# Performance work log

Measured on AMD Instinct MI355X. Metric: run time of the kernel, lower is better.

Reference implementation:

```python
import jax, jax.numpy as jnp
import numpy as np

N_HEAD = 16

def setup_inputs() -> dict:
    key = jax.random.key(0)
    ks = jax.random.split(key, 9)
    B, T, C = 4, 2048, 1024
    s = 0.02
    return {
        "x": jax.random.normal(ks[0], (B, T, C), dtype=jnp.float32),
        "Wq": jax.random.normal(ks[1], (C, C), dtype=jnp.float32) * s,
        "bq": jnp.zeros((C,), dtype=jnp.float32),
        "Wk": jax.random.normal(ks[2], (C, C), dtype=jnp.float32) * s,
        "bk": jnp.zeros((C,), dtype=jnp.float32),
        "Wv": jax.random.normal(ks[3], (C, C), dtype=jnp.float32) * s,
        "bv": jnp.zeros((C,), dtype=jnp.float32),
        "Wo": jax.random.normal(ks[4], (C, C), dtype=jnp.float32) * s,
        "bo": jnp.zeros((C,), dtype=jnp.float32),
    }

def reference(x, Wq, bq, Wk, bk, Wv, bv, Wo, bo):
    B, T, C = x.shape
    H = N_HEAD
    d = C // H
    # QKV projections (Linear: y = x @ W + b), split heads -> [B, H, T, d]
    def proj(W, b):
        return (x @ W + b).reshape(B, T, H, d).transpose(0, 2, 1, 3)
    q = proj(Wq, bq)
    k = proj(Wk, bk)
    v = proj(Wv, bv)
    scale = jnp.float32(d) ** -0.5
    scores = jnp.einsum("bhtd,bhsd->bhts", q, k) * scale  # [B,H,T,T]
    attn = jax.nn.softmax(scores, axis=-1)
    out = jnp.einsum("bhts,bhsd->bhtd", attn, v)  # [B,H,T,d]
    out = out.transpose(0, 2, 1, 3).reshape(B, T, C)
    return out @ Wo + bo
```

## Files before the change

kernel.cpp:

```cpp
#include <hip/hip_runtime.h>
#include <hip/hip_bf16.h>

typedef unsigned short u16;
typedef unsigned int   u32;

typedef __bf16 bf16x8 __attribute__((ext_vector_type(8)));
typedef float  f32x4  __attribute__((ext_vector_type(4)));

#define MFMA16(A, B, C) __builtin_amdgcn_mfma_f32_16x16x32_bf16(A, B, C, 0, 0, 0)

static __device__ __forceinline__ u16 f2bf(float f) {
  union { float f; u32 u; } v; v.f = f;
  u32 r = v.u + 0x7fffu + ((v.u >> 16) & 1u);
  return (u16)(r >> 16);
}

static __device__ __forceinline__ float exp2a(float x) {
  float r; asm("v_exp_f32 %0, %1" : "=v"(r) : "v"(x)); return r;
}
static __device__ __forceinline__ float max3f(float a, float b, float c) {
  float r; asm("v_max3_f32 %0, %1, %2, %3" : "=v"(r) : "v"(a), "v"(b), "v"(c)); return r;
}
static __device__ __forceinline__ u32 cvtpk(float lo, float hi) {
  u32 r; asm("v_cvt_pk_bf16_f32 %0, %1, %2" : "=v"(r) : "v"(lo), "v"(hi)); return r;
}

static __device__ __forceinline__ void async16(const void* g, void* l) {
  __builtin_amdgcn_global_load_lds((const __attribute__((address_space(1))) void*)g,
                                   (__attribute__((address_space(3))) void*)l, 16, 0, 0);
}

static __device__ __forceinline__ int permrow(int r) {
  return (r & 3) | (((r >> 3) & 1) << 2);
}

__global__ __launch_bounds__(256) void prep_k(const float* __restrict__ x, u16* __restrict__ xb,
                                              const float* __restrict__ Wq, const float* __restrict__ Wk,
                                              const float* __restrict__ Wv, const float* __restrict__ Wo,
                                              u16* __restrict__ WT) {
  __shared__ float tile[32][33];
  const int bid = blockIdx.x;
  if (bid < 8192) {
    size_t i = ((size_t)bid * 256 + threadIdx.x) * 4;
    float4 v = *(const float4*)(x + i);
    u32 lo = (u32)f2bf(v.x) | ((u32)f2bf(v.y) << 16);
    u32 hi = (u32)f2bf(v.z) | ((u32)f2bf(v.w) << 16);
    *(uint2*)(xb + i) = make_uint2(lo, hi);
  } else {
    const int rem = bid - 8192;
    const int z = rem >> 10;
    const int rr = rem & 1023;
    const int n0 = (rr & 31) * 32;
    const int k0 = (rr >> 5) * 32;
    const float* W = (z == 0) ? Wq : (z == 1) ? Wk : (z == 2) ? Wv : Wo;
    u16* out = WT + (size_t)z * 1048576;
    const int tx = threadIdx.x & 31, ty = threadIdx.x >> 5;
#pragma unroll
    for (int i = 0; i < 4; i++)
      tile[ty + i * 8][tx] = W[(size_t)(k0 + ty + i * 8) * 1024 + n0 + tx];
    __syncthreads();
#pragma unroll
    for (int i = 0; i < 4; i++)
      out[(size_t)(n0 + ty + i * 8) * 1024 + k0 + tx] = f2bf(tile[tx][ty + i * 8]);
  }
}

#define G_STAGE(NXT)                                                          \
  {                                                                           \
    async16(pgA0, &As[(NXT) * 16384 + (0 * 512 + tid) * 8]);                  \
    async16(pgA1, &As[(NXT) * 16384 + (1 * 512 + tid) * 8]);                  \
    async16(pgA2, &As[(NXT) * 16384 + (2 * 512 + tid) * 8]);                  \
    async16(pgA3, &As[(NXT) * 16384 + (3 * 512 + tid) * 8]);                  \
    async16(pgB0, &Bs[(NXT) * 8192 + (0 * 512 + tid) * 8]);                   \
    async16(pgB1, &Bs[(NXT) * 8192 + (1 * 512 + tid) * 8]);                   \
    pgA0 += 64; pgA1 += 64; pgA2 += 64; pgA3 += 64; pgB0 += 64; pgB1 += 64;   \
  }

#define COMPUTE_T(CUR)                                                        \
  _Pragma("unroll")                                                           \
  for (int kk = 0; kk < 2; ++kk) {                                            \
    const u16* pAk = kk ? pA1 : pA0;                                          \
    const u16* pBk = kk ? pB1 : pB0;                                          \
    bf16x8 a0 = *(const bf16x8*)(pAk + (CUR) * 16384);                        \
    bf16x8 a1 = *(const bf16x8*)(pAk + (CUR) * 16384 + 1024);                 \
    bf16x8 a2 = *(const bf16x8*)(pAk + (CUR) * 16384 + 2048);                 \
    bf16x8 a3 = *(const bf16x8*)(pAk + (CUR) * 16384 + 3072);                 \
    bf16x8 b0 = *(const bf16x8*)(pBk + (CUR) * 8192);                         \
    bf16x8 b1 = *(const bf16x8*)(pBk + (CUR) * 8192 + 1024);                  \
    bf16x8 b2 = *(const bf16x8*)(pBk + (CUR) * 8192 + 2048);                  \
    bf16x8 b3 = *(const bf16x8*)(pBk + (CUR) * 8192 + 3072);                  \
    __builtin_amdgcn_s_setprio(1);                                            \
    acc[0][0] = MFMA16(a0, b0, acc[0][0]); acc[0][1] = MFMA16(a0, b1, acc[0][1]); \
    acc[0][2] = MFMA16(a0, b2, acc[0][2]); acc[0][3] = MFMA16(a0, b3, acc[0][3]); \
    acc[1][0] = MFMA16(a1, b0, acc[1][0]); acc[1][1] = MFMA16(a1, b1, acc[1][1]); \
    acc[1][2] = MFMA16(a1, b2, acc[1][2]); acc[1][3] = MFMA16(a1, b3, acc[1][3]); \
    acc[2][0] = MFMA16(a2, b0, acc[2][0]); acc[2][1] = MFMA16(a2, b1, acc[2][1]); \
    acc[2][2] = MFMA16(a2, b2, acc[2][2]); acc[2][3] = MFMA16(a2, b3, acc[2][3]); \
    acc[3][0] = MFMA16(a3, b0, acc[3][0]); acc[3][1] = MFMA16(a3, b1, acc[3][1]); \
    acc[3][2] = MFMA16(a3, b2, acc[3][2]); acc[3][3] = MFMA16(a3, b3, acc[3][3]); \
    __builtin_amdgcn_s_setprio(0);                                            \
  }

#define GITER(CUR, WN, STG, NXT)                                              \
  {                                                                           \
    asm volatile("s_waitcnt vmcnt(" #WN ")" ::: "memory");                    \
    __builtin_amdgcn_s_barrier();                                             \
    __builtin_amdgcn_sched_barrier(0);                                        \
    if (STG) G_STAGE(NXT)                                                     \
    COMPUTE_T(CUR)                                                            \
  }

template <int MODE>
__global__ __launch_bounds__(512, 2) void gemm256_k(const u16* __restrict__ A, const u16* __restrict__ WTall,
                                                    const float* __restrict__ b0, const float* __restrict__ b1,
                                                    const float* __restrict__ b2,
                                                    u16* __restrict__ outb, float* __restrict__ outf) {
  __shared__ u16 As[3 * 16384];
  __shared__ u16 Bs[3 * 8192];
  const int tid = threadIdx.x;
  const int lane = tid & 63;
  const int wid = tid >> 6;
  const int wm = wid >> 1, wn = wid & 1;
  const int g = lane >> 4, cc = lane & 15;

  const int bid = blockIdx.x;
  const int xcd = bid & 7;
  const int idx = bid >> 3;
  const int m0 = (xcd * 4 + (idx & 3)) * 256;
  const int nb = (idx >> 2) * 128;
  const u16* Bg = WTall + (size_t)(MODE == 0 ? 0 : 3145728) + (size_t)nb * 1024;

  const u16* pgA0; const u16* pgA1; const u16* pgA2; const u16* pgA3;
  const u16* pgB0; const u16* pgB1;
  {
    const int u0 = tid, u1 = 512 + tid, u2 = 1024 + tid, u3 = 1536 + tid;
    pgA0 = A + (size_t)(m0 + (u0 >> 3)) * 1024 + (((u0 & 7) ^ ((u0 >> 3) & 7)) << 3);
    pgA1 = A + (size_t)(m0 + (u1 >> 3)) * 1024 + (((u1 & 7) ^ ((u1 >> 3) & 7)) << 3);
    pgA2 = A + (size_t)(m0 + (u2 >> 3)) * 1024 + (((u2 & 7) ^ ((u2 >> 3) & 7)) << 3);
    pgA3 = A + (size_t)(m0 + (u3 >> 3)) * 1024 + (((u3 & 7) ^ ((u3 >> 3) & 7)) << 3);
    pgB0 = Bg + (size_t)(u0 >> 3) * 1024 + (((u0 & 7) ^ ((u0 >> 3) & 7)) << 3);
    pgB1 = Bg + (size_t)(u1 >> 3) * 1024 + (((u1 & 7) ^ ((u1 >> 3) & 7)) << 3);
  }

  const int s0 = g ^ (cc & 7);
  const u16* pA0 = As + (wm * 64 + cc) * 64 + (s0 << 3);
  const u16* pA1 = As + (wm * 64 + cc) * 64 + ((s0 ^ 4) << 3);
  const u16* pB0 = Bs + (wn * 64 + cc) * 64 + (s0 << 3);
  const u16* pB1 = Bs + (wn * 64 + cc) * 64 + ((s0 ^ 4) << 3);

  f32x4 acc[4][4] = {};

  G_STAGE(0)
  G_STAGE(1)

  for (int to = 0; to < 12; to += 3) {
    GITER(0, 6, 1, 2)
    GITER(1, 6, 1, 0)
    GITER(2, 6, 1, 1)
  }
  GITER(0, 6, 1, 2)
  GITER(1, 6, 1, 0)
  GITER(2, 6, 0, 0)
  GITER(0, 0, 0, 0)

  const int z = (MODE == 0) ? (nb >> 10) : 0;
  const float* bias = (MODE == 0) ? (z == 0 ? b0 : (z == 1 ? b1 : b2)) : b0;
  const float scl = (MODE == 0 && z == 0) ? 0.18033688011112042f : 1.0f;

#pragma unroll
  for (int mi = 0; mi < 4; mi++) {
#pragma unroll
    for (int ni = 0; ni < 4; ni++) {
      const int ng = nb + wn * 64 + ni * 16 + cc;
      const int n = (MODE == 0) ? (ng & 1023) : ng;
      const float bn = bias[n];
      const int mb = m0 + wm * 64 + mi * 16 + g * 4;
      if (MODE == 0) {
        u16* o = outb + (size_t)z * 8388608;
        if (z == 2) {
          u16 h[4];
#pragma unroll
          for (int r = 0; r < 4; r++) h[r] = f2bf(acc[mi][ni][r] + bn);
          const size_t ix = ((size_t)(((mb >> 11) * 16 + (n >> 6)) * 64 + (n & 63))) * 2048 + (mb & 2047);
          *(uint2*)&o[ix] = make_uint2((u32)h[0] | ((u32)h[1] << 16), (u32)h[2] | ((u32)h[3] << 16));
        } else {
#pragma unroll
          for (int r = 0; r < 4; r++) {
            const int m = mb + r;
            const float val = (acc[mi][ni][r] + bn) * scl;
            o[((size_t)((m >> 11) * 16 + (n >> 6)) * 2048 + (m & 2047)) * 64 + (n & 63)] = f2bf(val);
          }
        }
      } else {
#pragma unroll
        for (int r = 0; r < 4; r++)
          outf[(size_t)(mb + r) * 1024 + n] = acc[mi][ni][r] + bn;
      }
    }
  }
}

#define SMAX(S0, S1, M, O, PF)                                                \
  {                                                                           \
    float pm_ = max3f(max3f(S0[0], S0[1], S0[2]),                             \
                      max3f(S0[3], S1[0], S1[1]), fmaxf(S1[2], S1[3]));       \
    if (__builtin_expect(!__all(pm_ <= M + 8.0f), 0)) {                       \
      pm_ = fmaxf(pm_, __shfl_xor(pm_, 16));                                  \
      pm_ = fmaxf(pm_, __shfl_xor(pm_, 32));                                  \
      const float mn_ = fmaxf(M, pm_);                                        \
      const float al_ = exp2a(M - mn_);                                       \
      _Pragma("unroll")                                                       \
      for (int r_ = 0; r_ < 4; ++r_) {                                        \
        const float ar_ = __shfl(al_, g * 4 + r_);                            \
        _Pragma("unroll")                                                     \
        for (int t_ = 0; t_ < 5; ++t_) O[t_][r_] *= ar_;                      \
      }                                                                       \
      M = mn_;                                                                \
    }                                                                         \
    const float e0_ = exp2a(S0[0] - M), e1_ = exp2a(S0[1] - M);               \
    const float e2_ = exp2a(S0[2] - M), e3_ = exp2a(S0[3] - M);               \
    const float e4_ = exp2a(S1[0] - M), e5_ = exp2a(S1[1] - M);               \
    const float e6_ = exp2a(S1[2] - M), e7_ = exp2a(S1[3] - M);               \
    union { u32 u[4]; bf16x8 v; } pu_;                                        \
    pu_.u[0] = cvtpk(e0_, e1_); pu_.u[1] = cvtpk(e2_, e3_);                   \
    pu_.u[2] = cvtpk(e4_, e5_); pu_.u[3] = cvtpk(e6_, e7_);                   \
    PF = pu_.v;                                                               \
  }

#define COMPUTE(KB, VB)                                                       \
  _Pragma("unroll")                                                           \
  for (int sub = 0; sub < 2; ++sub) {                                         \
    const u16* pV_ = sub ? pV1 : pV0;                                         \
    bf16x8 k00 = *(const bf16x8*)(pK0 + (KB)*4096 + sub*2048);                \
    bf16x8 k01 = *(const bf16x8*)(pK1 + (KB)*4096 + sub*2048);                \
    bf16x8 k10 = *(const bf16x8*)(pK0 + (KB)*4096 + sub*2048 + 256);          \
    bf16x8 k11 = *(const bf16x8*)(pK1 + (KB)*4096 + sub*2048 + 256);          \
    __builtin_amdgcn_s_setprio(1);                                            \
    f32x4 sA0 = {}, sA1 = {}, sB0 = {}, sB1 = {};                             \
    sA0 = MFMA16(k00, qfA[0], sA0); sA0 = MFMA16(k01, qfA[1], sA0);           \
    sB0 = MFMA16(k00, qfB[0], sB0); sB0 = MFMA16(k01, qfB[1], sB0);           \
    sA1 = MFMA16(k10, qfA[0], sA1); sA1 = MFMA16(k11, qfA[1], sA1);           \
    sB1 = MFMA16(k10, qfB[0], sB1); sB1 = MFMA16(k11, qfB[1], sB1);           \
    __builtin_amdgcn_s_setprio(0);                                            \
    bf16x8 pfA, pfB;                                                          \
    SMAX(sA0, sA1, mA, oA, pfA);                                              \
    SMAX(sB0, sB1, mB, oB, pfB);                                              \
    __builtin_amdgcn_s_setprio(1);                                            \
    _Pragma("unroll")                                                         \
    for (int t = 0; t < 4; ++t) {                                             \
      bf16x8 vf = *(const bf16x8*)(pV_ + (VB)*4096 + t*1024);                 \
      oA[t] = MFMA16(pfA, vf, oA[t]);                                         \
      oB[t] = MFMA16(pfB, vf, oB[t]);                                         \
    }                                                                         \
    oA[4] = MFMA16(pfA, vone, oA[4]);                                         \
    oB[4] = MFMA16(pfB, vone, oB[4]);                                         \
    __builtin_amdgcn_s_setprio(0);                                            \
  }

#define ASTEP(KB, VB, IT, WN, SK, SV, KSB, VSB)                               \
  {                                                                           \
    asm volatile("s_waitcnt vmcnt(" #WN ")" ::: "memory");                    \
    __builtin_amdgcn_s_barrier();                                             \
    __builtin_amdgcn_sched_barrier(0);                                        \
    if (SV) {                                                                 \
      const size_t vo_ = (size_t)((IT) + 1) * 64;                             \
      async16(vS0 + vo_, &Vs[(VSB) * 4096 + tid * 8]);                        \
      async16(vS1 + vo_, &Vs[(VSB) * 4096 + tid * 8 + 2048]);                 \
    }                                                                         \
    if (SK) {                                                                 \
      const size_t ko_ = (size_t)((IT) + 2) * 4096;                           \
      async16(kS0 + ko_, &Ks[(KSB) * 4096 + tid * 8]);                        \
      async16(kS1 + ko_, &Ks[(KSB) * 4096 + tid * 8 + 2048]);                 \
    }                                                                         \
    COMPUTE(KB, VB)                                                           \
  }

__global__ __launch_bounds__(256, 4) void attn_k(const u16* __restrict__ Qg, const u16* __restrict__ Kg,
                                                 const u16* __restrict__ Vtg, u16* __restrict__ ctx) {
  __shared__ u16 Ks[3 * 4096];
  __shared__ u16 Vs[2 * 4096];
  const int tid = threadIdx.x;
  const int lane = tid & 63;
  const int wid = tid >> 6;
  const int g = lane >> 4, cc = lane & 15;
  const int a_ = cc >> 2, b_ = cc & 3;

  const int bid = blockIdx.x;
  const int xcd = bid & 7, tt = bid >> 3;
  const int bh = xcd * 8 + (tt >> 4);
  const int q0 = (tt & 15) * 128 + wid * 16;
  const size_t base = (size_t)bh * 131072;

  bf16x8 qfA[2], qfB[2];
#pragma unroll
  for (int c2 = 0; c2 < 2; c2++) {
    qfA[c2] = *(const bf16x8*)(Qg + base + (size_t)(q0 + cc) * 64 + c2 * 32 + g * 8);
    qfB[c2] = *(const bf16x8*)(Qg + base + (size_t)(q0 + 64 + cc) * 64 + c2 * 32 + g * 8);
  }

  bf16x8 vone;
#pragma unroll
  for (int j = 0; j < 8; j++) vone[j] = (__bf16)1.0f;

  float mA = -30000.0f, mB = -30000.0f;
  f32x4 oA[5] = {}, oB[5] = {};

  const int cK = b_ | ((a_ & 1) << 2);
  const int slK = g ^ cK;
  const u16* pK0 = &Ks[(8 * a_ + b_) * 64 + (slK << 3)];
  const u16* pK1 = &Ks[(8 * a_ + b_) * 64 + ((slK ^ 4) << 3)];
  const int cV = b_ | (((cc >> 3) & 1) << 2);
  const u16* pV0 = &Vs[cc * 64 + ((g ^ cV) << 3)];
  const u16* pV1 = &Vs[cc * 64 + (((4 + g) ^ cV) << 3)];

  const int r0 = tid >> 3, r1 = r0 + 32;
  const int slot = tid & 7;
  const int sp0 = slot ^ permrow(r0), sp1 = slot ^ permrow(r1);
  const u16* kS0 = Kg + base + (size_t)r0 * 64 + (sp0 << 3);
  const u16* kS1 = Kg + base + (size_t)r1 * 64 + (sp1 << 3);
  const u16* vS0 = Vtg + base + (size_t)r0 * 2048 + (sp0 << 3);
  const u16* vS1 = Vtg + base + (size_t)r1 * 2048 + (sp1 << 3);

  async16(kS0, &Ks[tid * 8]);
  async16(kS1, &Ks[tid * 8 + 2048]);
  async16(vS0, &Vs[tid * 8]);
  async16(vS1, &Vs[tid * 8 + 2048]);
  async16(kS0 + 4096, &Ks[4096 + tid * 8]);
  async16(kS1 + 4096, &Ks[4096 + tid * 8 + 2048]);
  async16(vS0 + 64, &Vs[4096 + tid * 8]);
  async16(vS1 + 64, &Vs[4096 + tid * 8 + 2048]);

  ASTEP(0, 0, 0, 4, 1, 0, 2, 0)
  for (int itb = 1; itb <= 19; itb += 6) {
    ASTEP(1, 1, itb + 0, 2, 1, 1, 0, 0)
    ASTEP(2, 0, itb + 1, 2, 1, 1, 1, 1)
    ASTEP(0, 1, itb + 2, 2, 1, 1, 2, 0)
    ASTEP(1, 0, itb + 3, 2, 1, 1, 0, 1)
    ASTEP(2, 1, itb + 4, 2, 1, 1, 1, 0)
    ASTEP(0, 0, itb + 5, 2, 1, 1, 2, 1)
  }
  ASTEP(1, 1, 25, 2, 1, 1, 0, 0)
  ASTEP(2, 0, 26, 2, 1, 1, 1, 1)
  ASTEP(0, 1, 27, 2, 1, 1, 2, 0)
  ASTEP(1, 0, 28, 2, 1, 1, 0, 1)
  ASTEP(2, 1, 29, 2, 1, 1, 1, 0)
  ASTEP(0, 0, 30, 2, 0, 1, 0, 1)
  ASTEP(1, 1, 31, 0, 0, 0, 0, 0)

  const int b = bh >> 4, h = bh & 15;
#pragma unroll
  for (int r = 0; r < 4; r++) {
    {
      const float inv = __builtin_amdgcn_rcpf(oA[4][r]);
      const int q = q0 + g * 4 + r;
#pragma unroll
      for (int t = 0; t < 4; t++)
        ctx[((size_t)((b * 2048 + q) * 16 + h)) * 64 + t * 16 + cc] = f2bf(oA[t][r] * inv);
    }
    {
      const float inv = __builtin_amdgcn_rcpf(oB[4][r]);
      const int q = q0 + 64 + g * 4 + r;
#pragma unroll
      for (int t = 0; t < 4; t++)
        ctx[((size_t)((b * 2048 + q) * 16 + h)) * 64 + t * 16 + cc] = f2bf(oB[t][r] * inv);
    }
  }
}

extern "C" void kernel_launch(void* const* d_in, const int* in_sizes, int n_in,
                              void* d_out, int out_size, void* d_ws, size_t ws_size,
                              hipStream_t stream) {
  const float* x  = (const float*)d_in[0];
  const float* Wq = (const float*)d_in[1];
  const float* bq = (const float*)d_in[2];
  const float* Wk = (const float*)d_in[3];
  const float* bk = (const float*)d_in[4];
  const float* Wv = (const float*)d_in[5];
  const float* bv = (const float*)d_in[6];
  const float* Wo = (const float*)d_in[7];
  const float* bo = (const float*)d_in[8];
  float* out = (float*)d_out;

  char* w = (char*)d_ws;
  u16* xb   = (u16*)(w);
  u16* WT   = (u16*)(w + (16u << 20));
  u16* QKV  = (u16*)(w + (24u << 20));
  u16* ctxb = (u16*)(w + (72u << 20));

  prep_k<<<dim3(12288), dim3(256), 0, stream>>>(x, xb, Wq, Wk, Wv, Wo, WT);
  gemm256_k<0><<<dim3(768), dim3(512), 0, stream>>>(xb, WT, bq, bk, bv, QKV, nullptr);
  attn_k<<<dim3(1024), dim3(256), 0, stream>>>(QKV, QKV + 8388608, QKV + 2 * 8388608, ctxb);
  gemm256_k<1><<<dim3(256), dim3(512), 0, stream>>>(ctxb, WT, bo, nullptr, nullptr, nullptr, out);
}
```

Baseline: 176.2 us.

## Software-pipeline QK^T of next sub-tile with softmax and PV of current

```diff
diff --git a/kernel.cpp b/kernel.cpp
--- a/kernel.cpp
+++ b/kernel.cpp
@@ -227,28 +227,32 @@
     PF = pu_.v;                                                               \
   }
 
-#define COMPUTE(KB, VB)                                                       \
-  _Pragma("unroll")                                                           \
-  for (int sub = 0; sub < 2; ++sub) {                                         \
-    const u16* pV_ = sub ? pV1 : pV0;                                         \
-    bf16x8 k00 = *(const bf16x8*)(pK0 + (KB)*4096 + sub*2048);                \
-    bf16x8 k01 = *(const bf16x8*)(pK1 + (KB)*4096 + sub*2048);                \
-    bf16x8 k10 = *(const bf16x8*)(pK0 + (KB)*4096 + sub*2048 + 256);          \
-    bf16x8 k11 = *(const bf16x8*)(pK1 + (KB)*4096 + sub*2048 + 256);          \
+#define QKSUB(KB, SOFF, A0, A1, B0, B1)                                       \
+  {                                                                           \
+    bf16x8 k00 = *(const bf16x8*)(pK0 + (KB) * 4096 + (SOFF));                \
+    bf16x8 k01 = *(const bf16x8*)(pK1 + (KB) * 4096 + (SOFF));                \
+    bf16x8 k10 = *(const bf16x8*)(pK0 + (KB) * 4096 + (SOFF) + 256);          \
+    bf16x8 k11 = *(const bf16x8*)(pK1 + (KB) * 4096 + (SOFF) + 256);          \
     __builtin_amdgcn_s_setprio(1);                                            \
-    f32x4 sA0 = {}, sA1 = {}, sB0 = {}, sB1 = {};                             \
-    sA0 = MFMA16(k00, qfA[0], sA0); sA0 = MFMA16(k01, qfA[1], sA0);           \
-    sB0 = MFMA16(k00, qfB[0], sB0); sB0 = MFMA16(k01, qfB[1], sB0);           \
-    sA1 = MFMA16(k10, qfA[0], sA1); sA1 = MFMA16(k11, qfA[1], sA1);           \
-    sB1 = MFMA16(k10, qfB[0], sB1); sB1 = MFMA16(k11, qfB[1], sB1);           \
+    A0 = (f32x4){0.f, 0.f, 0.f, 0.f}; A1 = (f32x4){0.f, 0.f, 0.f, 0.f};      \
+    B0 = (f32x4){0.f, 0.f, 0.f, 0.f}; B1 = (f32x4){0.f, 0.f, 0.f, 0.f};      \
+    A0 = MFMA16(k00, qfA[0], A0); A0 = MFMA16(k01, qfA[1], A0);               \
+    B0 = MFMA16(k00, qfB[0], B0); B0 = MFMA16(k01, qfB[1], B0);               \
+    A1 = MFMA16(k10, qfA[0], A1); A1 = MFMA16(k11, qfA[1], A1);               \
+    B1 = MFMA16(k10, qfB[0], B1); B1 = MFMA16(k11, qfB[1], B1);               \
     __builtin_amdgcn_s_setprio(0);                                            \
+  }
+
+#define SMPV(A0, A1, B0, B1, VB, SUB)                                         \
+  {                                                                           \
     bf16x8 pfA, pfB;                                                          \
-    SMAX(sA0, sA1, mA, oA, pfA);                                              \
-    SMAX(sB0, sB1, mB, oB, pfB);                                              \
+    SMAX(A0, A1, mA, oA, pfA);                                                \
+    SMAX(B0, B1, mB, oB, pfB);                                                \
+    const u16* pV_ = (SUB) ? pV1 : pV0;                                       \
     __builtin_amdgcn_s_setprio(1);                                            \
     _Pragma("unroll")                                                         \
     for (int t = 0; t < 4; ++t) {                                             \
-      bf16x8 vf = *(const bf16x8*)(pV_ + (VB)*4096 + t*1024);                 \
+      bf16x8 vf = *(const bf16x8*)(pV_ + (VB) * 4096 + t * 1024);             \
       oA[t] = MFMA16(pfA, vf, oA[t]);                                         \
       oB[t] = MFMA16(pfB, vf, oB[t]);                                         \
     }                                                                         \
@@ -257,9 +261,9 @@
     __builtin_amdgcn_s_setprio(0);                                            \
   }
 
-#define ASTEP(KB, VB, IT, WN, SK, SV, KSB, VSB)                               \
-  {                                                                           \
-    asm volatile("s_waitcnt vmcnt(" #WN ")" ::: "memory");                    \
+#define ASTEP3(KB, KBN, VB, IT, WT, WM, SK, SV, KSB, VSB, DOQK)               \
+  {                                                                           \
+    asm volatile("s_waitcnt vmcnt(" #WT ")" ::: "memory");                    \
     __builtin_amdgcn_s_barrier();                                             \
     __builtin_amdgcn_sched_barrier(0);                                        \
     if (SV) {                                                                 \
@@ -272,7 +276,13 @@
       async16(kS0 + ko_, &Ks[(KSB) * 4096 + tid * 8]);                        \
       async16(kS1 + ko_, &Ks[(KSB) * 4096 + tid * 8 + 2048]);                 \
     }                                                                         \
-    COMPUTE(KB, VB)                                                           \
+    QKSUB((KB), 2048, yA0, yA1, yB0, yB1)                                     \
+    SMPV(xA0, xA1, xB0, xB1, VB, 0)                                           \
+    asm volatile("s_waitcnt vmcnt(" #WM ")" ::: "memory");                    \
+    __builtin_amdgcn_s_barrier();                                             \
+    __builtin_amdgcn_sched_barrier(0);                                        \
+    if (DOQK) QKSUB((KBN), 0, xA0, xA1, xB0, xB1)                             \
+    SMPV(yA0, yA1, yB0, yB1, VB, 1)                                           \
   }
 
 __global__ __launch_bounds__(256, 4) void attn_k(const u16* __restrict__ Qg, const u16* __restrict__ Kg,
@@ -304,6 +314,7 @@
 
   float mA = -30000.0f, mB = -30000.0f;
   f32x4 oA[5] = {}, oB[5] = {};
+  f32x4 xA0, xA1, xB0, xB1, yA0, yA1, yB0, yB1;
 
   const int cK = b_ | ((a_ & 1) << 2);
   const int slK = g ^ cK;
@@ -330,22 +341,27 @@
   async16(vS0 + 64, &Vs[4096 + tid * 8]);
   async16(vS1 + 64, &Vs[4096 + tid * 8 + 2048]);
 
-  ASTEP(0, 0, 0, 4, 1, 0, 2, 0)
+  asm volatile("s_waitcnt vmcnt(6)" ::: "memory");
+  __builtin_amdgcn_s_barrier();
+  __builtin_amdgcn_sched_barrier(0);
+  QKSUB(0, 0, xA0, xA1, xB0, xB1)
+
+  ASTEP3(0, 1, 0, 0, 4, 4, 1, 0, 2, 0, 1)
   for (int itb = 1; itb <= 19; itb += 6) {
-    ASTEP(1, 1, itb + 0, 2, 1, 1, 0, 0)
-    ASTEP(2, 0, itb + 1, 2, 1, 1, 1, 1)
-    ASTEP(0, 1, itb + 2, 2, 1, 1, 2, 0)
-    ASTEP(1, 0, itb + 3, 2, 1, 1, 0, 1)
-    ASTEP(2, 1, itb + 4, 2, 1, 1, 1, 0)
-    ASTEP(0, 0, itb + 5, 2, 1, 1, 2, 1)
-  }
-  ASTEP(1, 1, 25, 2, 1, 1, 0, 0)
-  ASTEP(2, 0, 26, 2, 1, 1, 1, 1)
-  ASTEP(0, 1, 27, 2, 1, 1, 2, 0)
-  ASTEP(1, 0, 28, 2, 1, 1, 0, 1)
-  ASTEP(2, 1, 29, 2, 1, 1, 1, 0)
-  ASTEP(0, 0, 30, 2, 0, 1, 0, 1)
-  ASTEP(1, 1, 31, 0, 0, 0, 0, 0)
+    ASTEP3(1, 2, 1, itb + 0, 2, 4, 1, 1, 0, 0, 1)
+    ASTEP3(2, 0, 0, itb + 1, 2, 4, 1, 1, 1, 1, 1)
+    ASTEP3(0, 1, 1, itb + 2, 2, 4, 1, 1, 2, 0, 1)
+    ASTEP3(1, 2, 0, itb + 3, 2, 4, 1, 1, 0, 1, 1)
+    ASTEP3(2, 0, 1, itb + 4, 2, 4, 1, 1, 1, 0, 1)
+    ASTEP3(0, 1, 0, itb + 5, 2, 4, 1, 1, 2, 1, 1)
+  }
+  ASTEP3(1, 2, 1, 25, 2, 4, 1, 1, 0, 0, 1)
+  ASTEP3(2, 0, 0, 26, 2, 4, 1, 1, 1, 1, 1)
+  ASTEP3(0, 1, 1, 27, 2, 4, 1, 1, 2, 0, 1)
+  ASTEP3(1, 2, 0, 28, 2, 4, 1, 1, 0, 1, 1)
+  ASTEP3(2, 0, 1, 29, 2, 4, 1, 1, 1, 0, 1)
+  ASTEP3(0, 1, 0, 30, 2, 2, 0, 1, 0, 1, 1)
+  ASTEP3(1, 2, 1, 31, 0, 0, 0, 0, 0, 0, 0)
 
   const int b = bh >> 4, h = bh & 15;
 #pragma unroll
```

Result: no change. 178.4 us (+1.3%).

## Rewrite projection GEMM as 4-wave 128x256 tile with split-stage pipelining

Applied to the files above, without the earlier changes.

```diff
diff --git a/kernel.cpp b/kernel.cpp
--- a/kernel.cpp
+++ b/kernel.cpp
@@ -65,136 +65,154 @@
   }
 }
 
-#define G_STAGE(NXT)                                                          \
-  {                                                                           \
-    async16(pgA0, &As[(NXT) * 16384 + (0 * 512 + tid) * 8]);                  \
-    async16(pgA1, &As[(NXT) * 16384 + (1 * 512 + tid) * 8]);                  \
-    async16(pgA2, &As[(NXT) * 16384 + (2 * 512 + tid) * 8]);                  \
-    async16(pgA3, &As[(NXT) * 16384 + (3 * 512 + tid) * 8]);                  \
-    async16(pgB0, &Bs[(NXT) * 8192 + (0 * 512 + tid) * 8]);                   \
-    async16(pgB1, &Bs[(NXT) * 8192 + (1 * 512 + tid) * 8]);                   \
-    pgA0 += 64; pgA1 += 64; pgA2 += 64; pgA3 += 64; pgB0 += 64; pgB1 += 64;   \
-  }
-
-#define COMPUTE_T(CUR)                                                        \
-  _Pragma("unroll")                                                           \
-  for (int kk = 0; kk < 2; ++kk) {                                            \
-    const u16* pAk = kk ? pA1 : pA0;                                          \
-    const u16* pBk = kk ? pB1 : pB0;                                          \
-    bf16x8 a0 = *(const bf16x8*)(pAk + (CUR) * 16384);                        \
-    bf16x8 a1 = *(const bf16x8*)(pAk + (CUR) * 16384 + 1024);                 \
-    bf16x8 a2 = *(const bf16x8*)(pAk + (CUR) * 16384 + 2048);                 \
-    bf16x8 a3 = *(const bf16x8*)(pAk + (CUR) * 16384 + 3072);                 \
-    bf16x8 b0 = *(const bf16x8*)(pBk + (CUR) * 8192);                         \
-    bf16x8 b1 = *(const bf16x8*)(pBk + (CUR) * 8192 + 1024);                  \
-    bf16x8 b2 = *(const bf16x8*)(pBk + (CUR) * 8192 + 2048);                  \
-    bf16x8 b3 = *(const bf16x8*)(pBk + (CUR) * 8192 + 3072);                  \
-    __builtin_amdgcn_s_setprio(1);                                            \
-    acc[0][0] = MFMA16(a0, b0, acc[0][0]); acc[0][1] = MFMA16(a0, b1, acc[0][1]); \
-    acc[0][2] = MFMA16(a0, b2, acc[0][2]); acc[0][3] = MFMA16(a0, b3, acc[0][3]); \
-    acc[1][0] = MFMA16(a1, b0, acc[1][0]); acc[1][1] = MFMA16(a1, b1, acc[1][1]); \
-    acc[1][2] = MFMA16(a1, b2, acc[1][2]); acc[1][3] = MFMA16(a1, b3, acc[1][3]); \
-    acc[2][0] = MFMA16(a2, b0, acc[2][0]); acc[2][1] = MFMA16(a2, b1, acc[2][1]); \
-    acc[2][2] = MFMA16(a2, b2, acc[2][2]); acc[2][3] = MFMA16(a2, b3, acc[2][3]); \
-    acc[3][0] = MFMA16(a3, b0, acc[3][0]); acc[3][1] = MFMA16(a3, b1, acc[3][1]); \
-    acc[3][2] = MFMA16(a3, b2, acc[3][2]); acc[3][3] = MFMA16(a3, b3, acc[3][3]); \
-    __builtin_amdgcn_s_setprio(0);                                            \
-  }
-
-#define GITER(CUR, WN, STG, NXT)                                              \
-  {                                                                           \
-    asm volatile("s_waitcnt vmcnt(" #WN ")" ::: "memory");                    \
-    __builtin_amdgcn_s_barrier();                                             \
-    __builtin_amdgcn_sched_barrier(0);                                        \
-    if (STG) G_STAGE(NXT)                                                     \
-    COMPUTE_T(CUR)                                                            \
-  }
+#define QMM(MB, NBA) { \
+  __builtin_amdgcn_s_setprio(1); \
+  _Pragma("unroll") for (int mf_ = 0; mf_ < 4; ++mf_) \
+    _Pragma("unroll") for (int nf_ = 0; nf_ < 2; ++nf_) { \
+      acc[(MB)+mf_][(NBA)+nf_] = MFMA16(aF[mf_][0], bF[(NBA)+nf_][0], acc[(MB)+mf_][(NBA)+nf_]); \
+      acc[(MB)+mf_][(NBA)+nf_] = MFMA16(aF[mf_][1], bF[(NBA)+nf_][1], acc[(MB)+mf_][(NBA)+nf_]); \
+    } \
+  __builtin_amdgcn_s_setprio(0); }
+
+#define QRDA(SL) \
+  _Pragma("unroll") for (int mf_ = 0; mf_ < 4; ++mf_) { \
+    aF[mf_][0] = *(const bf16x8*)(rA0 + (SL) * 4096 + mf_ * 1024); \
+    aF[mf_][1] = *(const bf16x8*)(rA1 + (SL) * 4096 + mf_ * 1024); }
+
+#define QRDB(SL, NBA) \
+  _Pragma("unroll") for (int nf_ = 0; nf_ < 2; ++nf_) { \
+    bF[(NBA)+nf_][0] = *(const bf16x8*)(rB0 + (SL) * 8192 + nf_ * 1024); \
+    bF[(NBA)+nf_][1] = *(const bf16x8*)(rB1 + (SL) * 8192 + nf_ * 1024); }
+
+#define QSTA(SL, KOFF) \
+  async16(pa0 + (KOFF), &As[(SL) * 4096 + tid * 8]); \
+  async16(pa1 + (KOFF), &As[(SL) * 4096 + (256 + tid) * 8]);
+
+#define QSTB(SL, NOFF) \
+  async16(pb0 + (NOFF), &Bs[(SL) * 8192 + tid * 8]); \
+  async16(pb1 + (NOFF), &Bs[(SL) * 8192 + (256 + tid) * 8]); \
+  async16(pb2 + (NOFF), &Bs[(SL) * 8192 + (512 + tid) * 8]); \
+  async16(pb3 + (NOFF), &Bs[(SL) * 8192 + (768 + tid) * 8]);
+
+#define QTILE(SA, SB, SC) \
+  pa0 += 64; pa1 += 64; pb0 += 64; pb1 += 64; pb2 += 64; pb3 += 64; \
+  asm volatile("s_waitcnt vmcnt(6)" ::: "memory"); \
+  __builtin_amdgcn_s_barrier(); __builtin_amdgcn_sched_barrier(0); \
+  QSTA(SC, 0) \
+  QRDA(SA) QRDB(SA, 0) \
+  QMM(0, 0) \
+  asm volatile("s_waitcnt vmcnt(2)" ::: "memory"); \
+  __builtin_amdgcn_s_barrier(); __builtin_amdgcn_sched_barrier(0); \
+  QSTB(SC, 0) \
+  QRDB(SB, 2) \
+  QMM(0, 2) \
+  asm volatile("s_waitcnt vmcnt(10)" ::: "memory"); \
+  __builtin_amdgcn_s_barrier(); __builtin_amdgcn_sched_barrier(0); \
+  QSTA(SA, 65536) \
+  QRDA(SB) \
+  QMM(4, 0) \
+  QSTB(SA, 32768) \
+  QMM(4, 2)
+
+#define QTAIL(SA, SB) \
+  asm volatile("s_waitcnt vmcnt(6)" ::: "memory"); \
+  __builtin_amdgcn_s_barrier(); __builtin_amdgcn_sched_barrier(0); \
+  QRDA(SA) QRDB(SA, 0) \
+  QMM(0, 0) \
+  asm volatile("s_waitcnt vmcnt(0)" ::: "memory"); \
+  __builtin_amdgcn_s_barrier(); __builtin_amdgcn_sched_barrier(0); \
+  QRDB(SB, 2) \
+  QMM(0, 2) \
+  QRDA(SB) \
+  QMM(4, 0) \
+  QMM(4, 2)
 
 template <int MODE>
-__global__ __launch_bounds__(512, 2) void gemm256_k(const u16* __restrict__ A, const u16* __restrict__ WTall,
-                                                    const float* __restrict__ b0, const float* __restrict__ b1,
-                                                    const float* __restrict__ b2,
-                                                    u16* __restrict__ outb, float* __restrict__ outf) {
-  __shared__ u16 As[3 * 16384];
+__global__ __launch_bounds__(256, 2) void qg8_k(const u16* __restrict__ A, const u16* __restrict__ WTall,
+                                                const float* __restrict__ b0, const float* __restrict__ b1,
+                                                const float* __restrict__ b2,
+                                                u16* __restrict__ outb, float* __restrict__ outf) {
+  __shared__ u16 As[3 * 4096];
   __shared__ u16 Bs[3 * 8192];
   const int tid = threadIdx.x;
   const int lane = tid & 63;
-  const int wid = tid >> 6;
-  const int wm = wid >> 1, wn = wid & 1;
+  const int wn = tid >> 6;
   const int g = lane >> 4, cc = lane & 15;
 
   const int bid = blockIdx.x;
   const int xcd = bid & 7;
   const int idx = bid >> 3;
-  const int m0 = (xcd * 4 + (idx & 3)) * 256;
-  const int nb = (idx >> 2) * 128;
+  const int m0 = (xcd * 8 + (idx & 7)) * 128;
+  const int nb = (idx >> 3) * 256;
   const u16* Bg = WTall + (size_t)(MODE == 0 ? 0 : 3145728) + (size_t)nb * 1024;
 
-  const u16* pgA0; const u16* pgA1; const u16* pgA2; const u16* pgA3;
-  const u16* pgB0; const u16* pgB1;
+  const u16* pa0; const u16* pa1;
+  const u16* pb0; const u16* pb1; const u16* pb2; const u16* pb3;
   {
-    const int u0 = tid, u1 = 512 + tid, u2 = 1024 + tid, u3 = 1536 + tid;
-    pgA0 = A + (size_t)(m0 + (u0 >> 3)) * 1024 + (((u0 & 7) ^ ((u0 >> 3) & 7)) << 3);
-    pgA1 = A + (size_t)(m0 + (u1 >> 3)) * 1024 + (((u1 & 7) ^ ((u1 >> 3) & 7)) << 3);
-    pgA2 = A + (size_t)(m0 + (u2 >> 3)) * 1024 + (((u2 & 7) ^ ((u2 >> 3) & 7)) << 3);
-    pgA3 = A + (size_t)(m0 + (u3 >> 3)) * 1024 + (((u3 & 7) ^ ((u3 >> 3) & 7)) << 3);
-    pgB0 = Bg + (size_t)(u0 >> 3) * 1024 + (((u0 & 7) ^ ((u0 >> 3) & 7)) << 3);
-    pgB1 = Bg + (size_t)(u1 >> 3) * 1024 + (((u1 & 7) ^ ((u1 >> 3) & 7)) << 3);
+    const int u0 = tid, u1 = 256 + tid;
+    pa0 = A + (size_t)(m0 + (u0 >> 3)) * 1024 + (((u0 & 7) ^ ((u0 >> 3) & 7)) << 3);
+    pa1 = A + (size_t)(m0 + (u1 >> 3)) * 1024 + (((u1 & 7) ^ ((u1 >> 3) & 7)) << 3);
+#define BPTR(U) (Bg + (size_t)((((U) >> 8) & 0x7fffffff) * 0 + (((U) >> 3) >> 5) * 64 + (((U) >> 3) & 31)) * 1024 + ((((U) & 7) ^ (((U) >> 3) & 7)) << 3))
+    pb0 = BPTR(tid);
+    pb1 = BPTR(256 + tid);
+    pb2 = BPTR(512 + tid);
+    pb3 = BPTR(768 + tid);
+#undef BPTR
   }
 
   const int s0 = g ^ (cc & 7);
-  const u16* pA0 = As + (wm * 64 + cc) * 64 + (s0 << 3);
-  const u16* pA1 = As + (wm * 64 + cc) * 64 + ((s0 ^ 4) << 3);
-  const u16* pB0 = Bs + (wn * 64 + cc) * 64 + (s0 << 3);
-  const u16* pB1 = Bs + (wn * 64 + cc) * 64 + ((s0 ^ 4) << 3);
-
-  f32x4 acc[4][4] = {};
-
-  G_STAGE(0)
-  G_STAGE(1)
-
-  for (int to = 0; to < 12; to += 3) {
-    GITER(0, 6, 1, 2)
-    GITER(1, 6, 1, 0)
-    GITER(2, 6, 1, 1)
-  }
-  GITER(0, 6, 1, 2)
-  GITER(1, 6, 1, 0)
-  GITER(2, 6, 0, 0)
-  GITER(0, 0, 0, 0)
+  const u16* rA0 = As + cc * 64 + (s0 << 3);
+  const u16* rA1 = As + cc * 64 + ((s0 ^ 4) << 3);
+  const u16* rB0 = Bs + (wn * 32 + cc) * 64 + (s0 << 3);
+  const u16* rB1 = Bs + (wn * 32 + cc) * 64 + ((s0 ^ 4) << 3);
+
+  f32x4 acc[8][4] = {};
+  bf16x8 aF[4][2], bF[4][2];
+
+  QSTA(0, 0)
+  QSTB(0, 0)
+  QSTA(1, 65536)
+  QSTB(1, 32768)
+
+  for (int rep = 0; rep < 5; ++rep) {
+    QTILE(0, 1, 2)
+    QTILE(2, 0, 1)
+    QTILE(1, 2, 0)
+  }
+  QTAIL(0, 1)
 
   const int z = (MODE == 0) ? (nb >> 10) : 0;
   const float* bias = (MODE == 0) ? (z == 0 ? b0 : (z == 1 ? b1 : b2)) : b0;
   const float scl = (MODE == 0 && z == 0) ? 0.18033688011112042f : 1.0f;
 
 #pragma unroll
-  for (int mi = 0; mi < 4; mi++) {
-#pragma unroll
-    for (int ni = 0; ni < 4; ni++) {
-      const int ng = nb + wn * 64 + ni * 16 + cc;
+  for (int mf = 0; mf < 8; mf++) {
+#pragma unroll
+    for (int nfa = 0; nfa < 4; nfa++) {
+      const int ng = nb + wn * 64 + nfa * 16 + cc;
       const int n = (MODE == 0) ? (ng & 1023) : ng;
       const float bn = bias[n];
-      const int mb = m0 + wm * 64 + mi * 16 + g * 4;
+      const int mb = m0 + mf * 16 + g * 4;
       if (MODE == 0) {
         u16* o = outb + (size_t)z * 8388608;
         if (z == 2) {
           u16 h[4];
 #pragma unroll
-          for (int r = 0; r < 4; r++) h[r] = f2bf(acc[mi][ni][r] + bn);
+          for (int r = 0; r < 4; r++) h[r] = f2bf(acc[mf][nfa][r] + bn);
           const size_t ix = ((size_t)(((mb >> 11) * 16 + (n >> 6)) * 64 + (n & 63))) * 2048 + (mb & 2047);
           *(uint2*)&o[ix] = make_uint2((u32)h[0] | ((u32)h[1] << 16), (u32)h[2] | ((u32)h[3] << 16));
         } else {
 #pragma unroll
           for (int r = 0; r < 4; r++) {
             const int m = mb + r;
-            const float val = (acc[mi][ni][r] + bn) * scl;
+            const float val = (acc[mf][nfa][r] + bn) * scl;
             o[((size_t)((m >> 11) * 16 + (n >> 6)) * 2048 + (m & 2047)) * 64 + (n & 63)] = f2bf(val);
           }
         }
       } else {
 #pragma unroll
         for (int r = 0; r < 4; r++)
-          outf[(size_t)(mb + r) * 1024 + n] = acc[mi][ni][r] + bn;
+          outf[(size_t)(mb + r) * 1024 + n] = acc[mf][nfa][r] + bn;
       }
     }
   }
@@ -388,7 +406,7 @@
   u16* ctxb = (u16*)(w + (72u << 20));
 
   prep_k<<<dim3(12288), dim3(256), 0, stream>>>(x, xb, Wq, Wk, Wv, Wo, WT);
-  gemm256_k<0><<<dim3(768), dim3(512), 0, stream>>>(xb, WT, bq, bk, bv, QKV, nullptr);
+  qg8_k<0><<<dim3(768), dim3(256), 0, stream>>>(xb, WT, bq, bk, bv, QKV, nullptr);
   attn_k<<<dim3(1024), dim3(256), 0, stream>>>(QKV, QKV + 8388608, QKV + 2 * 8388608, ctxb);
-  gemm256_k<1><<<dim3(256), dim3(512), 0, stream>>>(ctxb, WT, bo, nullptr, nullptr, nullptr, out);
-}
+  qg8_k<1><<<dim3(256), dim3(256), 0, stream>>>(ctxb, WT, bo, nullptr, nullptr, nullptr, out);
+}
```

Result: slower. 183.2 us (+4.0%).
